# Performance work log

Measured on AMD Instinct MI355X. Metric: run time of the kernel, lower is better.

The kernel has to match this reference:

```python
import jax, jax.numpy as jnp
import numpy as np

B = 2048
H = 4096
K = 4  # conv kernel size


def setup_inputs() -> dict:
    key = jax.random.key(0)
    ks = jax.random.split(key, 9)
    s = 1.0 / np.sqrt(H)
    x = jax.random.normal(ks[0], (B, H), dtype=jnp.float32)
    conv_state = jax.random.normal(ks[1], (B, H, K - 1), dtype=jnp.float32)
    rglru_state = jax.random.normal(ks[2], (B, H), dtype=jnp.float32)
    w_fused = jax.random.uniform(ks[3], (2 * H, H), jnp.float32, -s, s)
    conv_w = jax.random.uniform(ks[4], (H, K), jnp.float32, -0.5, 0.5)
    conv_b = jax.random.uniform(ks[5], (H,), jnp.float32, -0.5, 0.5)
    w_gates = jax.random.uniform(ks[6], (2 * H, H), jnp.float32, -s, s)
    a = jax.random.uniform(ks[7], (H,), jnp.float32, 0.5, 0.9)
    w_out = jax.random.uniform(ks[8], (H, H), jnp.float32, -s, s)
    return {"x": x, "conv_state": conv_state, "rglru_state": rglru_state,
            "w_fused": w_fused, "conv_w": conv_w, "conv_b": conv_b,
            "w_gates": w_gates, "a": a, "w_out": w_out}


def reference(x, conv_state, rglru_state, w_fused, conv_w, conv_b, w_gates, a, w_out):
    # fused input projection -> gate branch + recurrent branch
    fused = x @ w_fused.T                       # [B, 2H]
    gate_out, x_recur = fused[:, :H], fused[:, H:]
    gate = jax.nn.gelu(gate_out, approximate=False)

    # single-step causal depthwise conv
    xws = jnp.concatenate([conv_state, x_recur[:, :, None]], axis=-1)  # [B, H, K]
    x_conv = jnp.einsum('bhk,hk->bh', xws, conv_w) + conv_b            # [B, H]
    new_conv_state = xws[:, :, 1:]                                     # [B, H, K-1]

    # RG-LRU gates
    gates = x_conv @ w_gates.T                  # [B, 2H]
    i_t = jax.nn.sigmoid(gates[:, :H])
    r_t = jax.nn.sigmoid(gates[:, H:])
    a_t = jnp.exp(8.0 * r_t * jnp.log(a))       # a ** (8 * r_t), a > 0
    multiplier = jnp.sqrt(1.0 - a_t * a_t)
    new_rglru_state = rglru_state * a_t + multiplier * (i_t * x_conv)

    out = (gate * new_rglru_state) @ w_out.T    # [B, H]
    return out, new_conv_state, new_rglru_state
```

## Files before the change

### kernel.cpp

```cpp
#include <hip/hip_runtime.h>
#include <cstdint>
#include <cstddef>

#define HD   4096
#define BSZ  2048

constexpr int BM = 128, BN = 128, BKT = 64;

typedef __bf16 bf16x8 __attribute__((ext_vector_type(8)));
typedef float  f32x4  __attribute__((ext_vector_type(4)));

__device__ __forceinline__ unsigned short f2bf(float f) {
  unsigned u = __float_as_uint(f);
  u += 0x7fffu + ((u >> 16) & 1u);
  return (unsigned short)(u >> 16);
}
__device__ __forceinline__ float bf2f(unsigned short s) {
  return __uint_as_float(((unsigned)s) << 16);
}

#define AS1(p) ((__attribute__((address_space(1))) void*)(void*)(p))
#define AS3(p) ((__attribute__((address_space(3))) void*)(p))

__global__ void cvt_f32_to_bf16(const float4* __restrict__ src,
                                ushort4* __restrict__ dst, int n4) {
  int i = blockIdx.x * blockDim.x + threadIdx.x;
  if (i >= n4) return;
  float4 v = src[i];
  ushort4 o;
  o.x = f2bf(v.x); o.y = f2bf(v.y); o.z = f2bf(v.z); o.w = f2bf(v.w);
  dst[i] = o;
}

template <int MODE>
__global__ __launch_bounds__(256) void gemm_bt(
    const unsigned short* __restrict__ A, const unsigned short* __restrict__ Bw,
    float* __restrict__ outf, unsigned short* __restrict__ gate_bf,
    float* __restrict__ xrec, int M, int N, int K) {
  __shared__ unsigned short smA[BM * BKT];
  __shared__ unsigned short smB[BN * BKT];
  const int tid  = threadIdx.x;
  const int wid  = tid >> 6;
  const int lane = tid & 63;
  const int wm = wid >> 1, wn = wid & 1;
  const int l16 = lane & 15, q = lane >> 4;
  const int bx = blockIdx.x, by = blockIdx.y;
  const int srow = tid >> 3;
  const int scol = (((tid & 7) ^ ((tid >> 3) & 7)) * 8);
  const unsigned short* Ab = A + (size_t)(by * BM) * K + scol;
  const unsigned short* Bb = Bw + (size_t)(bx * BN) * K + scol;
  const int ldsbase = (wid * 8) * BKT;
  f32x4 acc[4][4] = {};

  for (int kt = 0; kt < K; kt += BKT) {
#pragma unroll
    for (int i = 0; i < 4; ++i) {
      __builtin_amdgcn_global_load_lds(AS1(Ab + (size_t)(i * 32 + srow) * K + kt),
                                       AS3(smA + i * 32 * BKT + ldsbase), 16, 0, 0);
      __builtin_amdgcn_global_load_lds(AS1(Bb + (size_t)(i * 32 + srow) * K + kt),
                                       AS3(smB + i * 32 * BKT + ldsbase), 16, 0, 0);
    }
    __syncthreads();
#pragma unroll
    for (int kk = 0; kk < BKT; kk += 32) {
      bf16x8 af[4], bfr[4];
#pragma unroll
      for (int i = 0; i < 4; ++i) {
        const int ar = wm * 64 + i * 16 + l16;
        af[i]  = *(const bf16x8*)(smA + ar * BKT + ((((kk >> 3) + q) ^ (ar & 7)) * 8));
      }
#pragma unroll
      for (int j = 0; j < 4; ++j) {
        const int br = wn * 64 + j * 16 + l16;
        bfr[j] = *(const bf16x8*)(smB + br * BKT + ((((kk >> 3) + q) ^ (br & 7)) * 8));
      }
#pragma unroll
      for (int i = 0; i < 4; ++i)
#pragma unroll
        for (int j = 0; j < 4; ++j)
          acc[i][j] = __builtin_amdgcn_mfma_f32_16x16x32_bf16(af[i], bfr[j], acc[i][j], 0, 0, 0);
    }
    __syncthreads();
  }

  const int gm0 = by * BM + wm * 64 + q * 4;
  const int gn0 = bx * BN + wn * 64 + l16;
#pragma unroll
  for (int i = 0; i < 4; ++i) {
#pragma unroll
    for (int j = 0; j < 4; ++j) {
      const int n = gn0 + j * 16;
#pragma unroll
      for (int r = 0; r < 4; ++r) {
        const int m = gm0 + i * 16 + r;
        float v = acc[i][j][r];
        if (MODE == 0) {
          outf[(size_t)m * N + n] = v;
        } else if (MODE == 2) {
          float s = 1.0f / (1.0f + expf(-v));
          gate_bf[(size_t)m * N + n] = f2bf(s);
        } else {
          if (n < HD) {
            float g = 0.5f * v * (1.0f + erff(v * 0.70710678118654752f));
            gate_bf[(size_t)m * HD + n] = f2bf(g);
          } else {
            xrec[(size_t)m * HD + (n - HD)] = v;
          }
        }
      }
    }
  }
}

__device__ __forceinline__ void stage_half(const unsigned short* src_rc, int ldg,
                                           int h, int kt, unsigned short* region,
                                           int wid) {
#pragma unroll
  for (int i = 0; i < 2; ++i)
    __builtin_amdgcn_global_load_lds(
        AS1(src_rc + (size_t)(h * 128 + i * 64) * ldg + kt * 64),
        AS3(region + wid * 8 * 64 + i * 64 * 64), 16, 0, 0);
}

template <int MODE>
__global__ __launch_bounds__(512) void gemm256(
    const unsigned short* __restrict__ A, const unsigned short* __restrict__ Bw,
    unsigned short* __restrict__ gate_bf, float* __restrict__ xrec,
    int N, int K) {
  __shared__ __align__(16) unsigned short sm[2][2][2][128 * 64];
  const int tid  = threadIdx.x;
  const int wid  = tid >> 6;
  const int lane = tid & 63;
  const int wm = wid >> 2, wn = wid & 3;
  const int l16 = lane & 15, q = lane >> 4;

  const int nx  = gridDim.x;
  const int lin = blockIdx.y * nx + blockIdx.x;
  const int swz = (lin & 7) * ((nx * gridDim.y) >> 3) + (lin >> 3);
  const int bx = swz % nx, by = swz / nx;

  const int srow   = tid >> 3;
  const int schunk = ((tid & 7) ^ (srow & 7)) * 8;
  const unsigned short* Asrc = A  + (size_t)(by * 256 + srow) * K + schunk;
  const unsigned short* Bsrc = Bw + (size_t)(bx * 256 + srow) * K + schunk;

  f32x4 acc[2][2][4][2] = {};
  const int NT = K >> 6;

  stage_half(Asrc, K, 0, 0, &sm[0][0][0][0], wid);
  stage_half(Bsrc, K, 0, 0, &sm[0][1][0][0], wid);
  stage_half(Bsrc, K, 1, 0, &sm[0][1][1][0], wid);
  stage_half(Asrc, K, 1, 0, &sm[0][0][1][0], wid);
  stage_half(Asrc, K, 0, 1, &sm[1][0][0][0], wid);
  stage_half(Bsrc, K, 0, 1, &sm[1][1][0][0], wid);
  asm volatile("s_waitcnt vmcnt(4)" ::: "memory");
  __builtin_amdgcn_s_barrier();

#define PHASE(QA, QB, STAGE_STMT)                                              \
  {                                                                            \
    const unsigned short* rgA = &sm[cur][0][QA][0];                            \
    const unsigned short* rgB = &sm[cur][1][QB][0];                            \
    bf16x8 a0[4], a1[4], b0[2], b1[2];                                         \
    _Pragma("unroll")                                                          \
    for (int i = 0; i < 4; ++i) {                                              \
      const int r = wm * 64 + i * 16 + l16;                                    \
      const int s = r & 7;                                                     \
      a0[i] = *(const bf16x8*)(rgA + r * 64 + ((q ^ s) << 3));                 \
      a1[i] = *(const bf16x8*)(rgA + r * 64 + (((4 + q) ^ s) << 3));           \
    }                                                                          \
    _Pragma("unroll")                                                          \
    for (int j = 0; j < 2; ++j) {                                              \
      const int r = wn * 32 + j * 16 + l16;                                    \
      const int s = r & 7;                                                     \
      b0[j] = *(const bf16x8*)(rgB + r * 64 + ((q ^ s) << 3));                 \
      b1[j] = *(const bf16x8*)(rgB + r * 64 + (((4 + q) ^ s) << 3));           \
    }                                                                          \
    STAGE_STMT;                                                                \
    __builtin_amdgcn_s_barrier();                                              \
    __builtin_amdgcn_s_setprio(1);                                             \
    _Pragma("unroll")                                                          \
    for (int i = 0; i < 4; ++i)                                                \
      _Pragma("unroll")                                                        \
      for (int j = 0; j < 2; ++j) {                                            \
        acc[QA][QB][i][j] = __builtin_amdgcn_mfma_f32_16x16x32_bf16(           \
            a0[i], b0[j], acc[QA][QB][i][j], 0, 0, 0);                         \
        acc[QA][QB][i][j] = __builtin_amdgcn_mfma_f32_16x16x32_bf16(           \
            a1[i], b1[j], acc[QA][QB][i][j], 0, 0, 0);                         \
      }                                                                        \
    __builtin_amdgcn_s_setprio(0);                                             \
  }

  for (int T = 0; T < NT; ++T) {
    const int cur = T & 1, nxt = cur ^ 1;
    PHASE(0, 0, if (T + 1 < NT) stage_half(Bsrc, K, 1, T + 1, &sm[nxt][1][1][0], wid))
    __builtin_amdgcn_s_barrier();
    PHASE(0, 1, if (T + 1 < NT) stage_half(Asrc, K, 1, T + 1, &sm[nxt][0][1][0], wid))
    __builtin_amdgcn_s_barrier();
    PHASE(1, 0, if (T + 2 < NT) stage_half(Asrc, K, 0, T + 2, &sm[cur][0][0][0], wid))
    __builtin_amdgcn_s_barrier();
    PHASE(1, 1, if (T + 2 < NT) stage_half(Bsrc, K, 0, T + 2, &sm[cur][1][0][0], wid))
    if (T < NT - 1) {
      if (T == NT - 2) asm volatile("s_waitcnt vmcnt(0)" ::: "memory");
      else             asm volatile("s_waitcnt vmcnt(4)" ::: "memory");
    }
    __builtin_amdgcn_s_barrier();
  }
#undef PHASE

  const int m0 = by * 256 + wm * 64 + q * 4;
  const int n0 = bx * 256 + wn * 32 + l16;
#pragma unroll
  for (int qa = 0; qa < 2; ++qa)
#pragma unroll
    for (int qb = 0; qb < 2; ++qb)
#pragma unroll
      for (int i = 0; i < 4; ++i)
#pragma unroll
        for (int j = 0; j < 2; ++j)
#pragma unroll
          for (int r = 0; r < 4; ++r) {
            const int m = m0 + qa * 128 + i * 16 + r;
            const int n = n0 + qb * 128 + j * 16;
            float v = acc[qa][qb][i][j][r];
            if (MODE == 2) {
              gate_bf[(size_t)m * N + n] = f2bf(1.0f / (1.0f + expf(-v)));
            } else {
              if (n < HD) {
                float g = 0.5f * v * (1.0f + erff(v * 0.70710678118654752f));
                gate_bf[(size_t)m * HD + n] = f2bf(g);
              } else {
                xrec[(size_t)m * HD + (n - HD)] = v;
              }
            }
          }
}

__global__ void conv_fuse(const float* __restrict__ cs, const float* xr,
                          const float4* __restrict__ cw, const float* __restrict__ cb,
                          float* __restrict__ ncs, float* xc_out,
                          unsigned short* __restrict__ xc_bf) {
  int t = blockIdx.x * 256 + threadIdx.x;
  int h = t & (HD - 1);
  float c0 = cs[3 * t + 0];
  float c1 = cs[3 * t + 1];
  float c2 = cs[3 * t + 2];
  float xv = xr[t];
  float4 w = cw[h];
  float v = fmaf(c0, w.x, fmaf(c1, w.y, fmaf(c2, w.z, fmaf(xv, w.w, cb[h]))));
  ncs[3 * t + 0] = c1;
  ncs[3 * t + 1] = c2;
  ncs[3 * t + 2] = xv;
  xc_out[t] = v;
  xc_bf[t] = f2bf(v);
}

__global__ void rglru_fuse(const unsigned short* __restrict__ gates_bf,
                           const float* __restrict__ av,
                           const float* __restrict__ rs, const float* __restrict__ xc,
                           const unsigned short* __restrict__ gbf,
                           float* __restrict__ nrs, unsigned short* __restrict__ gated) {
  int t = blockIdx.x * 256 + threadIdx.x;
  int h = t & (HD - 1);
  int b = t >> 12;
  float it = bf2f(gates_bf[(size_t)b * (2 * HD) + h]);
  float rt = bf2f(gates_bf[(size_t)b * (2 * HD) + HD + h]);
  float at = expf(8.0f * rt * logf(av[h]));
  float mult = sqrtf(fmaxf(0.0f, 1.0f - at * at));
  float x = xc[t];
  float nv = fmaf(rs[t], at, mult * (it * x));
  nrs[t] = nv;
  gated[t] = f2bf(bf2f(gbf[t]) * nv);
}

extern "C" void kernel_launch(void* const* d_in, const int* in_sizes, int n_in,
                              void* d_out, int out_size, void* d_ws, size_t ws_size,
                              hipStream_t stream) {
  const float* x  = (const float*)d_in[0];
  const float* cs = (const float*)d_in[1];
  const float* rs = (const float*)d_in[2];
  const float* wf = (const float*)d_in[3];
  const float* cw = (const float*)d_in[4];
  const float* cb = (const float*)d_in[5];
  const float* wg = (const float*)d_in[6];
  const float* av = (const float*)d_in[7];
  const float* wo = (const float*)d_in[8];

  float* out = (float*)d_out;
  float* ncs = out + (size_t)BSZ * HD;
  float* nrs = out + (size_t)BSZ * HD * 4;

  char* ws = (char*)d_ws;
  unsigned short* x_bf   = (unsigned short*)(ws);
  unsigned short* wf_bf  = (unsigned short*)(ws + (size_t)(16u)  * 1048576u);
  unsigned short* wg_bf  = (unsigned short*)(ws + (size_t)(80u)  * 1048576u);
  unsigned short* wo_bf  = (unsigned short*)(ws + (size_t)(144u) * 1048576u);
  unsigned short* gatebf = (unsigned short*)(ws + (size_t)(176u) * 1048576u);
  float*          xrc    = (float*)         (ws + (size_t)(192u) * 1048576u);
  unsigned short* xc_bf  = (unsigned short*)(ws + (size_t)(224u) * 1048576u);
  unsigned short* gates_bf = wf_bf;
  unsigned short* gated    = x_bf;

  cvt_f32_to_bf16<<<(BSZ * HD / 4) / 256, 256, 0, stream>>>((const float4*)x,  (ushort4*)x_bf,  BSZ * HD / 4);
  cvt_f32_to_bf16<<<(2 * HD * HD / 4) / 256, 256, 0, stream>>>((const float4*)wf, (ushort4*)wf_bf, 2 * HD * HD / 4);
  cvt_f32_to_bf16<<<(2 * HD * HD / 4) / 256, 256, 0, stream>>>((const float4*)wg, (ushort4*)wg_bf, 2 * HD * HD / 4);
  cvt_f32_to_bf16<<<(HD * HD / 4) / 256, 256, 0, stream>>>((const float4*)wo, (ushort4*)wo_bf, HD * HD / 4);

  dim3 g256(2 * HD / 256, BSZ / 256);
  gemm256<1><<<g256, 512, 0, stream>>>(x_bf, wf_bf, gatebf, xrc, 2 * HD, HD);
  conv_fuse<<<(BSZ * HD) / 256, 256, 0, stream>>>(cs, xrc, (const float4*)cw, cb, ncs, xrc, xc_bf);
  gemm256<2><<<g256, 512, 0, stream>>>(xc_bf, wg_bf, gates_bf, nullptr, 2 * HD, HD);
  rglru_fuse<<<(BSZ * HD) / 256, 256, 0, stream>>>(gates_bf, av, rs, xrc, gatebf, nrs, gated);
  dim3 g3(HD / BN, BSZ / BM);
  gemm_bt<0><<<g3, dim3(256), 0, stream>>>(gated, wo_bf, out, nullptr, nullptr, BSZ, HD, HD);
}
```

Measured before the change: 998.6 us.

## Restructure GEMM main loop to reuse fragments and request two blocks per CU

```diff
diff --git a/kernel.cpp b/kernel.cpp
--- a/kernel.cpp
+++ b/kernel.cpp
@@ -123,7 +123,7 @@
 }
 
 template <int MODE>
-__global__ __launch_bounds__(512) void gemm256(
+__global__ __launch_bounds__(512, 2) void gemm256(
     const unsigned short* __restrict__ A, const unsigned short* __restrict__ Bw,
     unsigned short* __restrict__ gate_bf, float* __restrict__ xrec,
     int N, int K) {
@@ -151,61 +151,95 @@
   stage_half(Bsrc, K, 0, 0, &sm[0][1][0][0], wid);
   stage_half(Bsrc, K, 1, 0, &sm[0][1][1][0], wid);
   stage_half(Asrc, K, 1, 0, &sm[0][0][1][0], wid);
-  stage_half(Asrc, K, 0, 1, &sm[1][0][0][0], wid);
-  stage_half(Bsrc, K, 0, 1, &sm[1][1][0][0], wid);
-  asm volatile("s_waitcnt vmcnt(4)" ::: "memory");
+  asm volatile("s_waitcnt vmcnt(2)" ::: "memory");
   __builtin_amdgcn_s_barrier();
-
-#define PHASE(QA, QB, STAGE_STMT)                                              \
-  {                                                                            \
-    const unsigned short* rgA = &sm[cur][0][QA][0];                            \
-    const unsigned short* rgB = &sm[cur][1][QB][0];                            \
-    bf16x8 a0[4], a1[4], b0[2], b1[2];                                         \
-    _Pragma("unroll")                                                          \
-    for (int i = 0; i < 4; ++i) {                                              \
-      const int r = wm * 64 + i * 16 + l16;                                    \
-      const int s = r & 7;                                                     \
-      a0[i] = *(const bf16x8*)(rgA + r * 64 + ((q ^ s) << 3));                 \
-      a1[i] = *(const bf16x8*)(rgA + r * 64 + (((4 + q) ^ s) << 3));           \
-    }                                                                          \
-    _Pragma("unroll")                                                          \
-    for (int j = 0; j < 2; ++j) {                                              \
-      const int r = wn * 32 + j * 16 + l16;                                    \
-      const int s = r & 7;                                                     \
-      b0[j] = *(const bf16x8*)(rgB + r * 64 + ((q ^ s) << 3));                 \
-      b1[j] = *(const bf16x8*)(rgB + r * 64 + (((4 + q) ^ s) << 3));           \
-    }                                                                          \
-    STAGE_STMT;                                                                \
-    __builtin_amdgcn_s_barrier();                                              \
-    __builtin_amdgcn_s_setprio(1);                                             \
-    _Pragma("unroll")                                                          \
-    for (int i = 0; i < 4; ++i)                                                \
-      _Pragma("unroll")                                                        \
-      for (int j = 0; j < 2; ++j) {                                            \
-        acc[QA][QB][i][j] = __builtin_amdgcn_mfma_f32_16x16x32_bf16(           \
-            a0[i], b0[j], acc[QA][QB][i][j], 0, 0, 0);                         \
-        acc[QA][QB][i][j] = __builtin_amdgcn_mfma_f32_16x16x32_bf16(           \
-            a1[i], b1[j], acc[QA][QB][i][j], 0, 0, 0);                         \
-      }                                                                        \
-    __builtin_amdgcn_s_setprio(0);                                             \
-  }
 
   for (int T = 0; T < NT; ++T) {
     const int cur = T & 1, nxt = cur ^ 1;
-    PHASE(0, 0, if (T + 1 < NT) stage_half(Bsrc, K, 1, T + 1, &sm[nxt][1][1][0], wid))
-    __builtin_amdgcn_s_barrier();
-    PHASE(0, 1, if (T + 1 < NT) stage_half(Asrc, K, 1, T + 1, &sm[nxt][0][1][0], wid))
-    __builtin_amdgcn_s_barrier();
-    PHASE(1, 0, if (T + 2 < NT) stage_half(Asrc, K, 0, T + 2, &sm[cur][0][0][0], wid))
-    __builtin_amdgcn_s_barrier();
-    PHASE(1, 1, if (T + 2 < NT) stage_half(Bsrc, K, 0, T + 2, &sm[cur][1][0][0], wid))
-    if (T < NT - 1) {
-      if (T == NT - 2) asm volatile("s_waitcnt vmcnt(0)" ::: "memory");
+    bf16x8 a[4][2], b0[2][2], b1[2][2];
+    {
+      const unsigned short* rgA  = &sm[cur][0][0][0];
+      const unsigned short* rgB0 = &sm[cur][1][0][0];
+      const unsigned short* rgB1 = &sm[cur][1][1][0];
+#pragma unroll
+      for (int j = 0; j < 2; ++j) {
+        const int r = wn * 32 + j * 16 + l16;
+        const int s = r & 7;
+        b0[j][0] = *(const bf16x8*)(rgB0 + r * 64 + ((q ^ s) << 3));
+        b0[j][1] = *(const bf16x8*)(rgB0 + r * 64 + (((4 + q) ^ s) << 3));
+        b1[j][0] = *(const bf16x8*)(rgB1 + r * 64 + ((q ^ s) << 3));
+        b1[j][1] = *(const bf16x8*)(rgB1 + r * 64 + (((4 + q) ^ s) << 3));
+      }
+#pragma unroll
+      for (int i = 0; i < 4; ++i) {
+        const int r = wm * 64 + i * 16 + l16;
+        const int s = r & 7;
+        a[i][0] = *(const bf16x8*)(rgA + r * 64 + ((q ^ s) << 3));
+        a[i][1] = *(const bf16x8*)(rgA + r * 64 + (((4 + q) ^ s) << 3));
+      }
+      if (T + 1 < NT) stage_half(Asrc, K, 0, T + 1, &sm[nxt][0][0][0], wid);
+      __builtin_amdgcn_s_barrier();
+      __builtin_amdgcn_s_setprio(1);
+#pragma unroll
+      for (int i = 0; i < 4; ++i)
+#pragma unroll
+        for (int j = 0; j < 2; ++j) {
+          acc[0][0][i][j] = __builtin_amdgcn_mfma_f32_16x16x32_bf16(a[i][0], b0[j][0], acc[0][0][i][j], 0, 0, 0);
+          acc[0][0][i][j] = __builtin_amdgcn_mfma_f32_16x16x32_bf16(a[i][1], b0[j][1], acc[0][0][i][j], 0, 0, 0);
+        }
+      __builtin_amdgcn_s_setprio(0);
+    }
+    {
+      if (T + 1 < NT) stage_half(Bsrc, K, 0, T + 1, &sm[nxt][1][0][0], wid);
+      if (T == NT - 1) asm volatile("s_waitcnt vmcnt(0)" ::: "memory");
       else             asm volatile("s_waitcnt vmcnt(4)" ::: "memory");
-    }
-    __builtin_amdgcn_s_barrier();
+      __builtin_amdgcn_s_barrier();
+      __builtin_amdgcn_s_setprio(1);
+#pragma unroll
+      for (int i = 0; i < 4; ++i)
+#pragma unroll
+        for (int j = 0; j < 2; ++j) {
+          acc[0][1][i][j] = __builtin_amdgcn_mfma_f32_16x16x32_bf16(a[i][0], b1[j][0], acc[0][1][i][j], 0, 0, 0);
+          acc[0][1][i][j] = __builtin_amdgcn_mfma_f32_16x16x32_bf16(a[i][1], b1[j][1], acc[0][1][i][j], 0, 0, 0);
+        }
+      __builtin_amdgcn_s_setprio(0);
+    }
+    {
+      const unsigned short* rgA = &sm[cur][0][1][0];
+#pragma unroll
+      for (int i = 0; i < 4; ++i) {
+        const int r = wm * 64 + i * 16 + l16;
+        const int s = r & 7;
+        a[i][0] = *(const bf16x8*)(rgA + r * 64 + ((q ^ s) << 3));
+        a[i][1] = *(const bf16x8*)(rgA + r * 64 + (((4 + q) ^ s) << 3));
+      }
+      if (T + 1 < NT) stage_half(Bsrc, K, 1, T + 1, &sm[nxt][1][1][0], wid);
+      __builtin_amdgcn_s_barrier();
+      __builtin_amdgcn_s_setprio(1);
+#pragma unroll
+      for (int i = 0; i < 4; ++i)
+#pragma unroll
+        for (int j = 0; j < 2; ++j) {
+          acc[1][0][i][j] = __builtin_amdgcn_mfma_f32_16x16x32_bf16(a[i][0], b0[j][0], acc[1][0][i][j], 0, 0, 0);
+          acc[1][0][i][j] = __builtin_amdgcn_mfma_f32_16x16x32_bf16(a[i][1], b0[j][1], acc[1][0][i][j], 0, 0, 0);
+        }
+      __builtin_amdgcn_s_setprio(0);
+    }
+    {
+      if (T + 1 < NT) stage_half(Asrc, K, 1, T + 1, &sm[nxt][0][1][0], wid);
+      asm volatile("s_waitcnt vmcnt(2)" ::: "memory");
+      __builtin_amdgcn_s_barrier();
+      __builtin_amdgcn_s_setprio(1);
+#pragma unroll
+      for (int i = 0; i < 4; ++i)
+#pragma unroll
+        for (int j = 0; j < 2; ++j) {
+          acc[1][1][i][j] = __builtin_amdgcn_mfma_f32_16x16x32_bf16(a[i][0], b1[j][0], acc[1][1][i][j], 0, 0, 0);
+          acc[1][1][i][j] = __builtin_amdgcn_mfma_f32_16x16x32_bf16(a[i][1], b1[j][1], acc[1][1][i][j], 0, 0, 0);
+        }
+      __builtin_amdgcn_s_setprio(0);
+    }
   }
-#undef PHASE
 
   const int m0 = by * 256 + wm * 64 + q * 4;
   const int n0 = bx * 256 + wn * 32 + l16;
```

New measurement: 895.8 us. 1.11x faster.

## Restructure 256x256 GEMM main loop with operand reuse and deeper prefetch

Applied to the files above, without the earlier changes.

```diff
diff --git a/kernel.cpp b/kernel.cpp
--- a/kernel.cpp
+++ b/kernel.cpp
@@ -123,7 +123,7 @@
 }
 
 template <int MODE>
-__global__ __launch_bounds__(512) void gemm256(
+__global__ __launch_bounds__(512, 2) void gemm256(
     const unsigned short* __restrict__ A, const unsigned short* __restrict__ Bw,
     unsigned short* __restrict__ gate_bf, float* __restrict__ xrec,
     int N, int K) {
@@ -147,65 +147,111 @@
   f32x4 acc[2][2][4][2] = {};
   const int NT = K >> 6;
 
+  bf16x8 a[4][2], b0[2][2], b1[2][2];
+
+#define BARX() __builtin_amdgcn_s_barrier()
+#define LGKM0() asm volatile("s_waitcnt lgkmcnt(0)" ::: "memory")
+#define READ_A(BUF, HALF)                                                      \
+  {                                                                            \
+    const unsigned short* rgA = &sm[BUF][0][HALF][0];                          \
+    _Pragma("unroll")                                                          \
+    for (int i = 0; i < 4; ++i) {                                              \
+      const int r = wm * 64 + i * 16 + l16;                                    \
+      const int s = r & 7;                                                     \
+      a[i][0] = *(const bf16x8*)(rgA + r * 64 + ((q ^ s) << 3));               \
+      a[i][1] = *(const bf16x8*)(rgA + r * 64 + (((4 + q) ^ s) << 3));         \
+    }                                                                          \
+  }
+#define READ_B(BUF, HALF, DST)                                                 \
+  {                                                                            \
+    const unsigned short* rgB = &sm[BUF][1][HALF][0];                          \
+    _Pragma("unroll")                                                          \
+    for (int j = 0; j < 2; ++j) {                                              \
+      const int r = wn * 32 + j * 16 + l16;                                    \
+      const int s = r & 7;                                                     \
+      DST[j][0] = *(const bf16x8*)(rgB + r * 64 + ((q ^ s) << 3));             \
+      DST[j][1] = *(const bf16x8*)(rgB + r * 64 + (((4 + q) ^ s) << 3));       \
+    }                                                                          \
+  }
+#define MFMA_Q(QA, QB, BB)                                                     \
+  __builtin_amdgcn_s_setprio(1);                                               \
+  _Pragma("unroll")                                                            \
+  for (int i = 0; i < 4; ++i)                                                  \
+    _Pragma("unroll")                                                          \
+    for (int j = 0; j < 2; ++j) {                                              \
+      acc[QA][QB][i][j] = __builtin_amdgcn_mfma_f32_16x16x32_bf16(             \
+          a[i][0], BB[j][0], acc[QA][QB][i][j], 0, 0, 0);                      \
+      acc[QA][QB][i][j] = __builtin_amdgcn_mfma_f32_16x16x32_bf16(             \
+          a[i][1], BB[j][1], acc[QA][QB][i][j], 0, 0, 0);                      \
+    }                                                                          \
+  __builtin_amdgcn_s_setprio(0)
+
   stage_half(Asrc, K, 0, 0, &sm[0][0][0][0], wid);
   stage_half(Bsrc, K, 0, 0, &sm[0][1][0][0], wid);
   stage_half(Bsrc, K, 1, 0, &sm[0][1][1][0], wid);
   stage_half(Asrc, K, 1, 0, &sm[0][0][1][0], wid);
   stage_half(Asrc, K, 0, 1, &sm[1][0][0][0], wid);
   stage_half(Bsrc, K, 0, 1, &sm[1][1][0][0], wid);
-  asm volatile("s_waitcnt vmcnt(4)" ::: "memory");
-  __builtin_amdgcn_s_barrier();
-
-#define PHASE(QA, QB, STAGE_STMT)                                              \
-  {                                                                            \
-    const unsigned short* rgA = &sm[cur][0][QA][0];                            \
-    const unsigned short* rgB = &sm[cur][1][QB][0];                            \
-    bf16x8 a0[4], a1[4], b0[2], b1[2];                                         \
-    _Pragma("unroll")                                                          \
-    for (int i = 0; i < 4; ++i) {                                              \
-      const int r = wm * 64 + i * 16 + l16;                                    \
-      const int s = r & 7;                                                     \
-      a0[i] = *(const bf16x8*)(rgA + r * 64 + ((q ^ s) << 3));                 \
-      a1[i] = *(const bf16x8*)(rgA + r * 64 + (((4 + q) ^ s) << 3));           \
-    }                                                                          \
-    _Pragma("unroll")                                                          \
-    for (int j = 0; j < 2; ++j) {                                              \
-      const int r = wn * 32 + j * 16 + l16;                                    \
-      const int s = r & 7;                                                     \
-      b0[j] = *(const bf16x8*)(rgB + r * 64 + ((q ^ s) << 3));                 \
-      b1[j] = *(const bf16x8*)(rgB + r * 64 + (((4 + q) ^ s) << 3));           \
-    }                                                                          \
-    STAGE_STMT;                                                                \
-    __builtin_amdgcn_s_barrier();                                              \
-    __builtin_amdgcn_s_setprio(1);                                             \
-    _Pragma("unroll")                                                          \
-    for (int i = 0; i < 4; ++i)                                                \
-      _Pragma("unroll")                                                        \
-      for (int j = 0; j < 2; ++j) {                                            \
-        acc[QA][QB][i][j] = __builtin_amdgcn_mfma_f32_16x16x32_bf16(           \
-            a0[i], b0[j], acc[QA][QB][i][j], 0, 0, 0);                         \
-        acc[QA][QB][i][j] = __builtin_amdgcn_mfma_f32_16x16x32_bf16(           \
-            a1[i], b1[j], acc[QA][QB][i][j], 0, 0, 0);                         \
-      }                                                                        \
-    __builtin_amdgcn_s_setprio(0);                                             \
-  }
-
-  for (int T = 0; T < NT; ++T) {
-    const int cur = T & 1, nxt = cur ^ 1;
-    PHASE(0, 0, if (T + 1 < NT) stage_half(Bsrc, K, 1, T + 1, &sm[nxt][1][1][0], wid))
-    __builtin_amdgcn_s_barrier();
-    PHASE(0, 1, if (T + 1 < NT) stage_half(Asrc, K, 1, T + 1, &sm[nxt][0][1][0], wid))
-    __builtin_amdgcn_s_barrier();
-    PHASE(1, 0, if (T + 2 < NT) stage_half(Asrc, K, 0, T + 2, &sm[cur][0][0][0], wid))
-    __builtin_amdgcn_s_barrier();
-    PHASE(1, 1, if (T + 2 < NT) stage_half(Bsrc, K, 0, T + 2, &sm[cur][1][0][0], wid))
-    if (T < NT - 1) {
-      if (T == NT - 2) asm volatile("s_waitcnt vmcnt(0)" ::: "memory");
-      else             asm volatile("s_waitcnt vmcnt(4)" ::: "memory");
-    }
-    __builtin_amdgcn_s_barrier();
-  }
-#undef PHASE
+  stage_half(Bsrc, K, 1, 1, &sm[1][1][1][0], wid);
+  asm volatile("s_waitcnt vmcnt(6)" ::: "memory");
+  BARX();
+
+  for (int it = 0; it < (NT >> 1); ++it) {
+    const int t1 = 2 * it + 1, t2 = 2 * it + 2, t3 = 2 * it + 3;
+    READ_A(0, 0); READ_B(0, 0, b0);
+    stage_half(Asrc, K, 1, t1, &sm[1][0][1][0], wid);
+    BARX(); LGKM0();
+    MFMA_Q(0, 0, b0);
+    BARX();
+    READ_B(0, 1, b1);
+    if (t2 < NT) stage_half(Asrc, K, 0, t2, &sm[0][0][0][0], wid);
+    BARX(); LGKM0();
+    MFMA_Q(0, 1, b1);
+    BARX();
+    READ_A(0, 1);
+    if (t2 < NT) stage_half(Bsrc, K, 0, t2, &sm[0][1][0][0], wid);
+    BARX(); LGKM0();
+    MFMA_Q(1, 0, b0);
+    BARX();
+    if (t2 < NT) {
+      stage_half(Bsrc, K, 1, t2, &sm[0][1][1][0], wid);
+      asm volatile("s_waitcnt vmcnt(6)" ::: "memory");
+    } else {
+      asm volatile("s_waitcnt vmcnt(0)" ::: "memory");
+    }
+    BARX();
+    MFMA_Q(1, 1, b1);
+    BARX();
+    READ_A(1, 0); READ_B(1, 0, b0);
+    if (t2 < NT) stage_half(Asrc, K, 1, t2, &sm[0][0][1][0], wid);
+    BARX(); LGKM0();
+    MFMA_Q(0, 0, b0);
+    BARX();
+    READ_B(1, 1, b1);
+    if (t3 < NT) stage_half(Asrc, K, 0, t3, &sm[1][0][0][0], wid);
+    BARX(); LGKM0();
+    MFMA_Q(0, 1, b1);
+    BARX();
+    READ_A(1, 1);
+    if (t3 < NT) stage_half(Bsrc, K, 0, t3, &sm[1][1][0][0], wid);
+    BARX(); LGKM0();
+    MFMA_Q(1, 0, b0);
+    BARX();
+    if (t3 < NT) {
+      stage_half(Bsrc, K, 1, t3, &sm[1][1][1][0], wid);
+      asm volatile("s_waitcnt vmcnt(6)" ::: "memory");
+    } else {
+      asm volatile("s_waitcnt vmcnt(0)" ::: "memory");
+    }
+    BARX();
+    MFMA_Q(1, 1, b1);
+    BARX();
+  }
+#undef MFMA_Q
+#undef READ_B
+#undef READ_A
+#undef LGKM0
+#undef BARX
 
   const int m0 = by * 256 + wm * 64 + q * 4;
   const int n0 = bx * 256 + wn * 32 + l16;
```

Measured after the change: 884.6 us. 11.4% less time.
